# Kernel optimization log

Hardware: AMD Instinct MI355X
Metric: run time of the kernel (lower is better)

## Reference

```python
import jax, jax.numpy as jnp
import numpy as np

N_NODES = 100000
N_EDGES = 320000
DIM = 128
BN_EPS = 1e-5
AGG_EPS = 1e-6


def setup_inputs() -> dict:
    key = jax.random.key(0)
    ks = jax.random.split(key, 12)
    s = 1.0 / np.sqrt(DIM)
    inp = {
        "x": jax.random.normal(ks[0], (N_NODES, DIM), dtype=jnp.float32),
        "e": jax.random.normal(ks[1], (N_EDGES, DIM), dtype=jnp.float32),
        "edge_index": jax.random.randint(ks[2], (2, N_EDGES), 0, N_NODES, dtype=jnp.int32),
        "Wa": jax.random.normal(ks[3], (DIM, DIM), dtype=jnp.float32) * s,
        "ba": jnp.zeros((DIM,), dtype=jnp.float32),
        "Wb": jax.random.normal(ks[4], (DIM, DIM), dtype=jnp.float32) * s,
        "bb": jnp.zeros((DIM,), dtype=jnp.float32),
        "Wd": jax.random.normal(ks[5], (DIM, DIM), dtype=jnp.float32) * s,
        "bd": jnp.zeros((DIM,), dtype=jnp.float32),
        "We": jax.random.normal(ks[6], (DIM, DIM), dtype=jnp.float32) * s,
        "be": jnp.zeros((DIM,), dtype=jnp.float32),
        "gamma": jnp.ones((DIM,), dtype=jnp.float32),
        "beta": jnp.zeros((DIM,), dtype=jnp.float32),
    }
    return inp


def reference(x, e, edge_index, Wa, ba, Wb, bb, Wd, bd, We, be, gamma, beta):
    # PyG source_to_target flow: j = edge_index[0] (source), i = edge_index[1] (target)
    src = edge_index[0]
    dst = edge_index[1]

    Ax = x @ Wa + ba
    Bx = x @ Wb + bb
    Dx = x @ Wd + bd
    Ex = x @ We + be

    # message: e_ij = Dx_i + Ex_j ; sigma = sigmoid(e_ij)  [n_edges, out_dim]
    e_ij = Dx[dst] + Ex[src]
    sigma = jax.nn.sigmoid(e_ij)

    # aggregate: gated mean over incoming edges of each target node
    num = jax.ops.segment_sum(sigma * Bx[src], dst, num_segments=N_NODES)
    den = jax.ops.segment_sum(sigma, dst, num_segments=N_NODES)
    aggr = num / (den + AGG_EPS)

    # update + BatchNorm (training stats, biased var) + ReLU; dropout=0, residual=False
    h = Ax + aggr
    mean = jnp.mean(h, axis=0)
    var = jnp.mean(jnp.square(h - mean), axis=0)
    h_norm = (h - mean) * jax.lax.rsqrt(var + BN_EPS)
    x_out = jax.nn.relu(gamma * h_norm + beta)

    # edge output is raw e_ij (bn_edge_e is never applied in forward)
    return x_out, e_ij
```

## Files before the change

kernel.cpp:

```cpp
#include <hip/hip_runtime.h>
#include <hip/hip_bf16.h>
#include <stdint.h>

#define N_NODES 100000
#define N_EDGES 320000
#define DIM 128
#define AGG_EPS 1e-6f
#define BN_EPS 1e-5f
#define NODE_BLOCKS 2048
#define SCAN_BLOCKS 391

typedef float f32x4 __attribute__((ext_vector_type(4)));
typedef float f32x2 __attribute__((ext_vector_type(2)));
typedef __bf16 bf16x8 __attribute__((ext_vector_type(8)));

__device__ __forceinline__ uint32_t f2bf(float f) {
  union { float f; uint32_t u; } v; v.f = f;
  uint32_t u = v.u;
  return (u + 0x7fffu + ((u >> 16) & 1u)) >> 16;
}
__device__ __forceinline__ float bf2f(uint32_t h) {
  union { uint32_t u; float f; } v; v.u = h << 16;
  return v.f;
}

__device__ __forceinline__ void nt_store2(float* p, float a, float b) {
  f32x2 v = {a, b};
  __builtin_nontemporal_store(v, (f32x2*)p);
}


__global__ __launch_bounds__(256) void k_prep(
    const float* __restrict__ Wa, const float* __restrict__ ba,
    const float* __restrict__ Wb, const float* __restrict__ bb,
    const float* __restrict__ Wd, const float* __restrict__ bd,
    const float* __restrict__ We, const float* __restrict__ be,
    ushort* __restrict__ wt, float* __restrict__ biasc,
    uint4* __restrict__ cnt_zero) {
  __shared__ float tile[64][65];
  const int tid = threadIdx.x;
  const int b = blockIdx.x;
  const int sel = b >> 2, tr = (b >> 1) & 1, tc = b & 1;
  const float* W = (sel == 0) ? Wa : (sel == 1) ? Wb : (sel == 2) ? Wd : We;
#pragma unroll
  for (int i = 0; i < 16; ++i) {
    int idx = tid + 256 * i;
    int lr = idx >> 6, lc = idx & 63;
    tile[lr][lc] = W[(tr * 64 + lr) * 128 + tc * 64 + lc];
  }
  __syncthreads();
#pragma unroll
  for (int i = 0; i < 16; ++i) {
    int idx = tid + 256 * i;
    int oc = idx >> 6, ok = idx & 63;
    wt[(sel * 128 + tc * 64 + oc) * 128 + tr * 64 + ok] = (ushort)f2bf(tile[ok][oc]);
  }
  if (b == 0) {
    for (int t = tid; t < 512; t += 256) {
      int s2 = t >> 7;
      const float* bp = (s2 == 0) ? ba : (s2 == 1) ? bb : (s2 == 2) ? bd : be;
      biasc[t] = bp[t & 127];
    }
  }
  for (int j = b * 256 + tid; j < 25000; j += 16 * 256)
    cnt_zero[j] = make_uint4(0u, 0u, 0u, 0u);
}

__global__ __launch_bounds__(256) void k_gemm(
    const float* __restrict__ x, const ushort* __restrict__ wt,
    const float* __restrict__ biasc, ushort* __restrict__ abde) {
  __shared__ ushort As[128 * 128];
  __shared__ ushort Bs[64 * 128];
  const int tid = threadIdx.x;
  const int m0 = blockIdx.x * 128;

#pragma unroll
  for (int i = 0; i < 8; ++i) {
    int qid = tid + 256 * i;
    int row = qid >> 4, q = qid & 15;
    int gr = m0 + row;
    uint4 pk = make_uint4(0u, 0u, 0u, 0u);
    if (gr < N_NODES) {
      const float* s = x + (size_t)gr * 128 + q * 8;
      float4 f0 = *(const float4*)(s);
      float4 f1 = *(const float4*)(s + 4);
      pk.x = f2bf(f0.x) | (f2bf(f0.y) << 16);
      pk.y = f2bf(f0.z) | (f2bf(f0.w) << 16);
      pk.z = f2bf(f1.x) | (f2bf(f1.y) << 16);
      pk.w = f2bf(f1.z) | (f2bf(f1.w) << 16);
    }
    int byte = (row * 256 + q * 16) ^ ((row & 7) << 4);
    *(uint4*)((char*)As + byte) = pk;
  }
  __syncthreads();

  const int w = tid >> 6, lane = tid & 63;
  const int r = lane & 15, g = lane >> 4;

  bf16x8 afrag[2][4];
#pragma unroll
  for (int m = 0; m < 2; ++m)
#pragma unroll
    for (int kk = 0; kk < 4; ++kk) {
      int arow = w * 32 + m * 16 + r;
      int ab = (arow * 256 + kk * 64 + g * 16) ^ ((arow & 7) << 4);
      afrag[m][kk] = *(const bf16x8*)((const char*)As + ab);
    }

  const int ntpair[4][2] = {{2, 6}, {3, 7}, {0, 4}, {1, 5}};
  for (int ph = 0; ph < 4; ++ph) {
    f32x4 acc[2][2][4] = {};
#pragma unroll
    for (int t2 = 0; t2 < 2; ++t2) {
      if (ph | t2) __syncthreads();
      const int n0 = ntpair[ph][t2] * 64;
#pragma unroll
      for (int i = 0; i < 4; ++i) {
        int qid = tid + 256 * i;
        int row = qid >> 4, q = qid & 15;
        uint4 v = *(const uint4*)(wt + (n0 + row) * 128 + q * 8);
        int byte = (row * 256 + q * 16) ^ ((row & 7) << 4);
        *(uint4*)((char*)Bs + byte) = v;
      }
      __syncthreads();
#pragma unroll
      for (int kk = 0; kk < 4; ++kk) {
        bf16x8 bv[4];
#pragma unroll
        for (int n = 0; n < 4; ++n) {
          int brow = n * 16 + r;
          int bb = (brow * 256 + kk * 64 + g * 16) ^ ((brow & 7) << 4);
          bv[n] = *(const bf16x8*)((const char*)Bs + bb);
        }
#pragma unroll
        for (int m = 0; m < 2; ++m)
#pragma unroll
          for (int n = 0; n < 4; ++n)
            acc[t2][m][n] = __builtin_amdgcn_mfma_f32_16x16x32_bf16(
                afrag[m][kk], bv[n], acc[t2][m][n], 0, 0, 0);
      }
    }
#pragma unroll
    for (int t2 = 0; t2 < 2; ++t2) {
#pragma unroll
      for (int m = 0; m < 2; ++m) {
#pragma unroll
        for (int n = 0; n < 4; ++n) {
          int lc = t2 * 64 + n * 16 + r;
          float bsv = biasc[ntpair[ph][t2] * 64 + n * 16 + r];
#pragma unroll
          for (int q = 0; q < 4; ++q) {
            int row = w * 32 + m * 16 + g * 4 + q;
            As[row * 128 + (lc ^ (((row >> 2) & 3) << 4))] =
                (ushort)f2bf(acc[t2][m][n][q] + bsv);
          }
        }
      }
    }
    __syncthreads();
#pragma unroll
    for (int it = 0; it < 8; ++it) {
      int u = tid + 256 * it;
      int row = u >> 4, mq = u & 15;
      int xo = ((row >> 2) & 3) << 4;
      uint2 lo = *(const uint2*)&As[row * 128 + ((4 * mq) ^ xo)];
      uint2 hi = *(const uint2*)&As[row * 128 + ((64 + 4 * mq) ^ xo)];
      uint4 val = (ph < 2) ? make_uint4(hi.x, lo.x, hi.y, lo.y)
                           : make_uint4(lo.x, hi.x, lo.y, hi.y);
      int gr = m0 + row;
      if (gr < N_NODES)
        *(uint4*)((char*)abde + (size_t)gr * 1024 + (ph * 16 + mq) * 16) = val;
    }
  }
}

__global__ __launch_bounds__(256) void k_count(const int* __restrict__ dst,
                                               int* __restrict__ cnt) {
  int t = blockIdx.x * 256 + threadIdx.x;
  if (t < N_EDGES) atomicAdd(&cnt[dst[t]], 1);
}

__global__ __launch_bounds__(256) void k_bsum(const int* __restrict__ cnt,
                                              int* __restrict__ bsum2) {
  __shared__ int lds[256];
  int t = threadIdx.x;
  int i = blockIdx.x * 256 + t;
  lds[t] = (i < N_NODES) ? cnt[i] : 0;
  __syncthreads();
#pragma unroll
  for (int off = 128; off > 0; off >>= 1) {
    if (t < off) lds[t] += lds[t + off];
    __syncthreads();
  }
  if (t == 0) bsum2[blockIdx.x] = lds[0];
}

__global__ __launch_bounds__(256) void k_scan(const int* __restrict__ cnt,
                                              const int* __restrict__ bsum2,
                                              int* __restrict__ row_ptr,
                                              int* __restrict__ cursor) {
  __shared__ int ps[256];
  __shared__ int lds[256];
  __shared__ int boff_s;
  const int t = threadIdx.x;
  int a = (2 * t < SCAN_BLOCKS) ? bsum2[2 * t] : 0;
  int b = (2 * t + 1 < SCAN_BLOCKS) ? bsum2[2 * t + 1] : 0;
  ps[t] = a + b;
  __syncthreads();
  for (int off = 1; off < 256; off <<= 1) {
    int v = (t >= off) ? ps[t - off] : 0;
    __syncthreads();
    ps[t] += v;
    __syncthreads();
  }
  if (t == 0) {
    int b0 = blockIdx.x, p = b0 >> 1;
    int pre = (p > 0) ? ps[p - 1] : 0;
    if (b0 & 1) pre += bsum2[b0 - 1];
    boff_s = pre;
  }
  int i = blockIdx.x * 256 + t;
  int v = (i < N_NODES) ? cnt[i] : 0;
  lds[t] = v;
  __syncthreads();
  for (int off = 1; off < 256; off <<= 1) {
    int u = (t >= off) ? lds[t - off] : 0;
    __syncthreads();
    lds[t] += u;
    __syncthreads();
  }
  if (i < N_NODES) {
    int ex = boff_s + lds[t] - v;
    row_ptr[i] = ex;
    cursor[i] = ex;
  }
  if (blockIdx.x == 0 && t == 0) row_ptr[N_NODES] = N_EDGES;
}

__global__ __launch_bounds__(256) void k_scatter(const int* __restrict__ dst,
                                                 const int* __restrict__ srcArr,
                                                 int* __restrict__ cursor,
                                                 int* __restrict__ csr_eid,
                                                 int* __restrict__ csr_src) {
  int t = blockIdx.x * 256 + threadIdx.x;
  if (t < N_EDGES) {
    int d = dst[t];
    int s = srcArr[t];
    int pos = atomicAdd(&cursor[d], 1);
    csr_eid[pos] = t;
    csr_src[pos] = s;
  }
}

__global__ __launch_bounds__(256) void k_node(
    const ushort* __restrict__ abde, const int* __restrict__ row_ptr,
    const int* __restrict__ csr_eid, const int* __restrict__ csr_src,
    float* __restrict__ out_e, ushort* __restrict__ h,
    float* __restrict__ partials) {
  const int tid = threadIdx.x;
  const int lane = tid & 63;
  const int wid = (blockIdx.x << 2) | (tid >> 6);
  const int nw = NODE_BLOCKS * 4;
  float s0 = 0.f, s1 = 0.f, q0 = 0.f, q1 = 0.f;

  int i = wid;
  int k0 = 0, ke = 0;
  uint2 ad = make_uint2(0u, 0u);
  if (i < N_NODES) {
    k0 = row_ptr[i];
    ke = row_ptr[i + 1];
    ad = *(const uint2*)((const char*)abde + (size_t)i * 1024 + 512 + lane * 8);
  }
  while (i < N_NODES) {
    const int inext = i + nw;
    int nk0 = 0, nke = 0;
    uint2 nad = make_uint2(0u, 0u);
    if (inext < N_NODES) {
      nk0 = row_ptr[inext];
      nke = row_ptr[inext + 1];
      nad = *(const uint2*)((const char*)abde + (size_t)inext * 1024 + 512 + lane * 8);
    }
    float ax0 = bf2f(ad.x & 0xffffu), ax1 = bf2f(ad.x >> 16);
    float dx0 = bf2f(ad.y & 0xffffu), dx1 = bf2f(ad.y >> 16);
    float n0 = 0.f, n1 = 0.f, d0 = 0.f, d1 = 0.f;
    for (int base = k0; base < ke; base += 64) {
      const int cnt = min(64, ke - base);
      int eidv = 0, srcv = 0;
      if (lane < cnt) {
        eidv = csr_eid[base + lane];
        srcv = csr_src[base + lane];
      }
      int j = 0;
      for (; j + 2 <= cnt; j += 2) {
        int eA = __shfl(eidv, j),     sA = __shfl(srcv, j);
        int eB = __shfl(eidv, j + 1), sB = __shfl(srcv, j + 1);
        uint2 ebA = *(const uint2*)((const char*)abde + (size_t)sA * 1024 + lane * 8);
        uint2 ebB = *(const uint2*)((const char*)abde + (size_t)sB * 1024 + lane * 8);
        float e0 = dx0 + bf2f(ebA.x & 0xffffu);
        float e1 = dx1 + bf2f(ebA.x >> 16);
        nt_store2(out_e + (size_t)eA * 128 + 2 * lane, e0, e1);
        float sg0 = 1.f / (1.f + __expf(-e0));
        float sg1 = 1.f / (1.f + __expf(-e1));
        n0 += sg0 * bf2f(ebA.y & 0xffffu); n1 += sg1 * bf2f(ebA.y >> 16);
        d0 += sg0; d1 += sg1;
        float f0 = dx0 + bf2f(ebB.x & 0xffffu);
        float f1 = dx1 + bf2f(ebB.x >> 16);
        nt_store2(out_e + (size_t)eB * 128 + 2 * lane, f0, f1);
        float tg0 = 1.f / (1.f + __expf(-f0));
        float tg1 = 1.f / (1.f + __expf(-f1));
        n0 += tg0 * bf2f(ebB.y & 0xffffu); n1 += tg1 * bf2f(ebB.y >> 16);
        d0 += tg0; d1 += tg1;
      }
      if (j < cnt) {
        int eA = __shfl(eidv, j), sA = __shfl(srcv, j);
        uint2 ebA = *(const uint2*)((const char*)abde + (size_t)sA * 1024 + lane * 8);
        float e0 = dx0 + bf2f(ebA.x & 0xffffu);
        float e1 = dx1 + bf2f(ebA.x >> 16);
        nt_store2(out_e + (size_t)eA * 128 + 2 * lane, e0, e1);
        float sg0 = 1.f / (1.f + __expf(-e0));
        float sg1 = 1.f / (1.f + __expf(-e1));
        n0 += sg0 * bf2f(ebA.y & 0xffffu); n1 += sg1 * bf2f(ebA.y >> 16);
        d0 += sg0; d1 += sg1;
      }
    }
    float h0 = ax0 + n0 / (d0 + AGG_EPS);
    float h1 = ax1 + n1 / (d1 + AGG_EPS);
    *(uint32_t*)(h + (size_t)i * 128 + 2 * lane) = f2bf(h0) | (f2bf(h1) << 16);
    s0 += h0; s1 += h1; q0 += h0 * h0; q1 += h1 * h1;
    i = inext; k0 = nk0; ke = nke; ad = nad;
  }
  __shared__ float red[256 * 4];
  red[tid] = s0; red[256 + tid] = s1; red[512 + tid] = q0; red[768 + tid] = q1;
  __syncthreads();
  if (tid < 64) {
    float vs0 = red[tid] + red[tid + 64] + red[tid + 128] + red[tid + 192];
    float vs1 = red[256 + tid] + red[256 + tid + 64] + red[256 + tid + 128] + red[256 + tid + 192];
    float vq0 = red[512 + tid] + red[512 + tid + 64] + red[512 + tid + 128] + red[512 + tid + 192];
    float vq1 = red[768 + tid] + red[768 + tid + 64] + red[768 + tid + 128] + red[768 + tid + 192];
    float* p = partials + blockIdx.x * 256;
    p[2 * tid] = vs0;
    p[2 * tid + 1] = vs1;
    p[128 + 2 * tid] = vq0;
    p[128 + 2 * tid + 1] = vq1;
  }
}

__global__ __launch_bounds__(256) void k_stats1(const float* __restrict__ partials,
                                                float* __restrict__ out2) {
  int t = threadIdx.x, b = blockIdx.x;
  float s = 0.f;
#pragma unroll
  for (int j = 0; j < 32; ++j) s += partials[(b * 32 + j) * 256 + t];
  out2[b * 256 + t] = s;
}

__global__ __launch_bounds__(128) void k_stats2(const float* __restrict__ out2,
                                                float* __restrict__ stats) {
  int c = threadIdx.x;
  float s = 0.f, q = 0.f;
#pragma unroll
  for (int b = 0; b < 64; ++b) {
    s += out2[b * 256 + c];
    q += out2[b * 256 + 128 + c];
  }
  float mean = s * (1.f / (float)N_NODES);
  float var = q * (1.f / (float)N_NODES) - mean * mean;
  stats[c] = mean;
  stats[128 + c] = rsqrtf(var + BN_EPS);
}

__global__ __launch_bounds__(256) void k_final(const ushort* __restrict__ h,
    const float* __restrict__ gamma, const float* __restrict__ beta,
    const float* __restrict__ stats, float* __restrict__ out_x) {
  int idx = blockIdx.x * 256 + threadIdx.x;
  int c = (idx & 15) * 8;
  uint4 hv = *(const uint4*)(h + idx * 8);
  uint32_t hw[4] = {hv.x, hv.y, hv.z, hv.w};
  float out[8];
#pragma unroll
  for (int j = 0; j < 8; ++j) {
    uint32_t u = (j & 1) ? (hw[j >> 1] >> 16) : (hw[j >> 1] & 0xffffu);
    float hf = bf2f(u);
    int cc = c + j;
    float v = gamma[cc] * (hf - stats[cc]) * stats[128 + cc] + beta[cc];
    out[j] = fmaxf(v, 0.f);
  }
  f32x4 v0 = {out[0], out[1], out[2], out[3]};
  f32x4 v1 = {out[4], out[5], out[6], out[7]};
  __builtin_nontemporal_store(v0, (f32x4*)(out_x + idx * 8));
  __builtin_nontemporal_store(v1, (f32x4*)(out_x + idx * 8 + 4));
}

extern "C" void kernel_launch(void* const* d_in, const int* in_sizes, int n_in,
                              void* d_out, int out_size, void* d_ws, size_t ws_size,
                              hipStream_t stream) {
  const float* x = (const float*)d_in[0];
  const int* edge_index = (const int*)d_in[2];
  const float* Wa = (const float*)d_in[3];
  const float* ba = (const float*)d_in[4];
  const float* Wb = (const float*)d_in[5];
  const float* bb = (const float*)d_in[6];
  const float* Wd = (const float*)d_in[7];
  const float* bd = (const float*)d_in[8];
  const float* We = (const float*)d_in[9];
  const float* be = (const float*)d_in[10];
  const float* gamma = (const float*)d_in[11];
  const float* beta = (const float*)d_in[12];

  const int* src = edge_index;
  const int* dst = edge_index + N_EDGES;

  char* w = (char*)d_ws;
  ushort* wt      = (ushort*)(w);
  float*  biasc   = (float*)(w + 131072);
  ushort* abde    = (ushort*)(w + 133120);
  ushort* hbuf    = (ushort*)(w + 102533120);
  int*    cnt     = (int*)(w + 128133120);
  int*    row_ptr = (int*)(w + 128533120);
  int*    cursor  = (int*)(w + 128933248);
  int*    csr_eid = (int*)(w + 129333248);
  float*  partials= (float*)(w + 130613248);
  float*  stats   = (float*)(w + 132710400);

  int*   bsum2 = (int*)partials;
  float* out2  = (float*)cnt;

  float* out_x = (float*)d_out;
  float* out_e = out_x + (size_t)N_NODES * DIM;
  int* csr_src = (int*)out_x;

  k_prep<<<16, 256, 0, stream>>>(Wa, ba, Wb, bb, Wd, bd, We, be, wt, biasc, (uint4*)cnt);
  k_gemm<<<782, 256, 0, stream>>>(x, wt, biasc, abde);
  k_count<<<(N_EDGES + 255) / 256, 256, 0, stream>>>(dst, cnt);
  k_bsum<<<SCAN_BLOCKS, 256, 0, stream>>>(cnt, bsum2);
  k_scan<<<SCAN_BLOCKS, 256, 0, stream>>>(cnt, bsum2, row_ptr, cursor);
  k_scatter<<<(N_EDGES + 255) / 256, 256, 0, stream>>>(dst, src, cursor, csr_eid, csr_src);
  k_node<<<NODE_BLOCKS, 256, 0, stream>>>(abde, row_ptr, csr_eid, csr_src, out_e, hbuf, partials);
  k_stats1<<<64, 256, 0, stream>>>(partials, out2);
  k_stats2<<<1, 128, 0, stream>>>(out2, stats);
  k_final<<<6250, 256, 0, stream>>>(hbuf, gamma, beta, stats, out_x);
}
```

Measured before the change: 176.0 us.

## Fuse CSR build and BN stats kernels to cut launch count

Edge counting moves into extra blocks of the GEMM launch so both run concurrently. Block-sum, scan and scatter are merged into one cooperative kernel that uses grid-wide syncs. The two stats kernels become one, where the last-arriving block (found through an atomic ticket) computes mean and rstd. This removes several kernel launches and their gaps, but adds grid-sync overhead and requires all 1250 cooperative blocks to be co-resident.

```diff
diff --git a/kernel.cpp b/kernel.cpp
--- a/kernel.cpp
+++ b/kernel.cpp
@@ -1,6 +1,9 @@
 #include <hip/hip_runtime.h>
 #include <hip/hip_bf16.h>
+#include <hip/hip_cooperative_groups.h>
 #include <stdint.h>
+
+namespace cg = cooperative_groups;
 
 #define N_NODES 100000
 #define N_EDGES 320000
@@ -9,6 +12,8 @@
 #define BN_EPS 1e-5f
 #define NODE_BLOCKS 2048
 #define SCAN_BLOCKS 391
+#define GEMM_BLOCKS 782
+#define EDGE_BLOCKS 1250
 
 typedef float f32x4 __attribute__((ext_vector_type(4)));
 typedef float f32x2 __attribute__((ext_vector_type(2)));
@@ -23,7 +28,6 @@
   union { uint32_t u; float f; } v; v.u = h << 16;
   return v.f;
 }
-
 __device__ __forceinline__ void nt_store2(float* p, float a, float b) {
   f32x2 v = {a, b};
   __builtin_nontemporal_store(v, (f32x2*)p);
@@ -36,7 +40,7 @@
     const float* __restrict__ Wd, const float* __restrict__ bd,
     const float* __restrict__ We, const float* __restrict__ be,
     ushort* __restrict__ wt, float* __restrict__ biasc,
-    uint4* __restrict__ cnt_zero) {
+    uint4* __restrict__ cnt_zero, int* __restrict__ done) {
   __shared__ float tile[64][65];
   const int tid = threadIdx.x;
   const int b = blockIdx.x;
@@ -61,18 +65,27 @@
       const float* bp = (s2 == 0) ? ba : (s2 == 1) ? bb : (s2 == 2) ? bd : be;
       biasc[t] = bp[t & 127];
     }
+    if (tid == 0) *done = 0;
   }
   for (int j = b * 256 + tid; j < 25000; j += 16 * 256)
     cnt_zero[j] = make_uint4(0u, 0u, 0u, 0u);
 }
 
-__global__ __launch_bounds__(256) void k_gemm(
+__global__ __launch_bounds__(256) void k_gemm_count(
     const float* __restrict__ x, const ushort* __restrict__ wt,
-    const float* __restrict__ biasc, ushort* __restrict__ abde) {
+    const float* __restrict__ biasc, ushort* __restrict__ abde,
+    const int* __restrict__ dst, int* __restrict__ cnt) {
   __shared__ ushort As[128 * 128];
   __shared__ ushort Bs[64 * 128];
   const int tid = threadIdx.x;
-  const int m0 = blockIdx.x * 128;
+  const int bid = blockIdx.x;
+
+  if (bid >= GEMM_BLOCKS) {
+    int e = (bid - GEMM_BLOCKS) * 256 + tid;
+    if (e < N_EDGES) atomicAdd(&cnt[dst[e]], 1);
+    return;
+  }
+  const int m0 = bid * 128;
 
 #pragma unroll
   for (int i = 0; i < 8; ++i) {
@@ -174,80 +187,73 @@
   }
 }
 
-__global__ __launch_bounds__(256) void k_count(const int* __restrict__ dst,
-                                               int* __restrict__ cnt) {
-  int t = blockIdx.x * 256 + threadIdx.x;
-  if (t < N_EDGES) atomicAdd(&cnt[dst[t]], 1);
-}
-
-__global__ __launch_bounds__(256) void k_bsum(const int* __restrict__ cnt,
-                                              int* __restrict__ bsum2) {
-  __shared__ int lds[256];
-  int t = threadIdx.x;
-  int i = blockIdx.x * 256 + t;
-  lds[t] = (i < N_NODES) ? cnt[i] : 0;
-  __syncthreads();
-#pragma unroll
-  for (int off = 128; off > 0; off >>= 1) {
-    if (t < off) lds[t] += lds[t + off];
-    __syncthreads();
-  }
-  if (t == 0) bsum2[blockIdx.x] = lds[0];
-}
-
-__global__ __launch_bounds__(256) void k_scan(const int* __restrict__ cnt,
-                                              const int* __restrict__ bsum2,
-                                              int* __restrict__ row_ptr,
-                                              int* __restrict__ cursor) {
+__global__ __launch_bounds__(256) void k_csr(
+    const int* __restrict__ dst, const int* __restrict__ srcArr,
+    const int* __restrict__ cnt, int* __restrict__ bsum2,
+    int* __restrict__ row_ptr, int* __restrict__ cursor,
+    int* __restrict__ csr_eid, int* __restrict__ csr_src) {
+  cg::grid_group grid = cg::this_grid();
   __shared__ int ps[256];
   __shared__ int lds[256];
   __shared__ int boff_s;
   const int t = threadIdx.x;
-  int a = (2 * t < SCAN_BLOCKS) ? bsum2[2 * t] : 0;
-  int b = (2 * t + 1 < SCAN_BLOCKS) ? bsum2[2 * t + 1] : 0;
-  ps[t] = a + b;
-  __syncthreads();
-  for (int off = 1; off < 256; off <<= 1) {
-    int v = (t >= off) ? ps[t - off] : 0;
+  const int b = blockIdx.x;
+
+  if (b < SCAN_BLOCKS) {
+    int i = b * 256 + t;
+    lds[t] = (i < N_NODES) ? cnt[i] : 0;
     __syncthreads();
-    ps[t] += v;
+#pragma unroll
+    for (int off = 128; off > 0; off >>= 1) {
+      if (t < off) lds[t] += lds[t + off];
+      __syncthreads();
+    }
+    if (t == 0) bsum2[b] = lds[0];
+  }
+  grid.sync();
+
+  if (b < SCAN_BLOCKS) {
+    int a = (2 * t < SCAN_BLOCKS) ? bsum2[2 * t] : 0;
+    int bb = (2 * t + 1 < SCAN_BLOCKS) ? bsum2[2 * t + 1] : 0;
+    ps[t] = a + bb;
     __syncthreads();
-  }
-  if (t == 0) {
-    int b0 = blockIdx.x, p = b0 >> 1;
-    int pre = (p > 0) ? ps[p - 1] : 0;
-    if (b0 & 1) pre += bsum2[b0 - 1];
-    boff_s = pre;
-  }
-  int i = blockIdx.x * 256 + t;
-  int v = (i < N_NODES) ? cnt[i] : 0;
-  lds[t] = v;
-  __syncthreads();
-  for (int off = 1; off < 256; off <<= 1) {
-    int u = (t >= off) ? lds[t - off] : 0;
+    for (int off = 1; off < 256; off <<= 1) {
+      int v = (t >= off) ? ps[t - off] : 0;
+      __syncthreads();
+      ps[t] += v;
+      __syncthreads();
+    }
+    if (t == 0) {
+      int p = b >> 1;
+      int pre = (p > 0) ? ps[p - 1] : 0;
+      if (b & 1) pre += bsum2[b - 1];
+      boff_s = pre;
+    }
+    int i = b * 256 + t;
+    int v = (i < N_NODES) ? cnt[i] : 0;
+    lds[t] = v;
     __syncthreads();
-    lds[t] += u;
-    __syncthreads();
-  }
-  if (i < N_NODES) {
-    int ex = boff_s + lds[t] - v;
-    row_ptr[i] = ex;
-    cursor[i] = ex;
-  }
-  if (blockIdx.x == 0 && t == 0) row_ptr[N_NODES] = N_EDGES;
-}
-
-__global__ __launch_bounds__(256) void k_scatter(const int* __restrict__ dst,
-                                                 const int* __restrict__ srcArr,
-                                                 int* __restrict__ cursor,
-                                                 int* __restrict__ csr_eid,
-                                                 int* __restrict__ csr_src) {
-  int t = blockIdx.x * 256 + threadIdx.x;
-  if (t < N_EDGES) {
-    int d = dst[t];
-    int s = srcArr[t];
+    for (int off = 1; off < 256; off <<= 1) {
+      int u = (t >= off) ? lds[t - off] : 0;
+      __syncthreads();
+      lds[t] += u;
+      __syncthreads();
+    }
+    if (i < N_NODES) {
+      int ex = boff_s + lds[t] - v;
+      row_ptr[i] = ex;
+      cursor[i] = ex;
+    }
+    if (b == 0 && t == 0) row_ptr[N_NODES] = N_EDGES;
+  }
+  grid.sync();
+
+  int e = b * 256 + t;
+  if (e < N_EDGES) {
+    int d = dst[e];
+    int s = srcArr[e];
     int pos = atomicAdd(&cursor[d], 1);
-    csr_eid[pos] = t;
+    csr_eid[pos] = e;
     csr_src[pos] = s;
   }
 }
@@ -345,28 +351,31 @@
   }
 }
 
-__global__ __launch_bounds__(256) void k_stats1(const float* __restrict__ partials,
-                                                float* __restrict__ out2) {
-  int t = threadIdx.x, b = blockIdx.x;
+__global__ __launch_bounds__(256) void k_stats(const float* __restrict__ partials,
+                                               float* __restrict__ out2,
+                                               float* __restrict__ stats,
+                                               int* __restrict__ done) {
+  const int t = threadIdx.x, b = blockIdx.x;
   float s = 0.f;
 #pragma unroll
   for (int j = 0; j < 32; ++j) s += partials[(b * 32 + j) * 256 + t];
   out2[b * 256 + t] = s;
-}
-
-__global__ __launch_bounds__(128) void k_stats2(const float* __restrict__ out2,
-                                                float* __restrict__ stats) {
-  int c = threadIdx.x;
-  float s = 0.f, q = 0.f;
-#pragma unroll
-  for (int b = 0; b < 64; ++b) {
-    s += out2[b * 256 + c];
-    q += out2[b * 256 + 128 + c];
-  }
-  float mean = s * (1.f / (float)N_NODES);
-  float var = q * (1.f / (float)N_NODES) - mean * mean;
-  stats[c] = mean;
-  stats[128 + c] = rsqrtf(var + BN_EPS);
+  __threadfence();
+  __shared__ int ticket;
+  if (t == 0) ticket = atomicAdd(done, 1);
+  __syncthreads();
+  if (ticket == 63 && t < 128) {
+    float ss = 0.f, qq = 0.f;
+#pragma unroll
+    for (int bb = 0; bb < 64; ++bb) {
+      ss += out2[bb * 256 + t];
+      qq += out2[bb * 256 + 128 + t];
+    }
+    float mean = ss * (1.f / (float)N_NODES);
+    float var = qq * (1.f / (float)N_NODES) - mean * mean;
+    stats[t] = mean;
+    stats[128 + t] = rsqrtf(var + BN_EPS);
+  }
 }
 
 __global__ __launch_bounds__(256) void k_final(const ushort* __restrict__ h,
@@ -424,19 +433,22 @@
 
   int*   bsum2 = (int*)partials;
   float* out2  = (float*)cnt;
+  int*   done  = row_ptr + 100001;
 
   float* out_x = (float*)d_out;
   float* out_e = out_x + (size_t)N_NODES * DIM;
   int* csr_src = (int*)out_x;
 
-  k_prep<<<16, 256, 0, stream>>>(Wa, ba, Wb, bb, Wd, bd, We, be, wt, biasc, (uint4*)cnt);
-  k_gemm<<<782, 256, 0, stream>>>(x, wt, biasc, abde);
-  k_count<<<(N_EDGES + 255) / 256, 256, 0, stream>>>(dst, cnt);
-  k_bsum<<<SCAN_BLOCKS, 256, 0, stream>>>(cnt, bsum2);
-  k_scan<<<SCAN_BLOCKS, 256, 0, stream>>>(cnt, bsum2, row_ptr, cursor);
-  k_scatter<<<(N_EDGES + 255) / 256, 256, 0, stream>>>(dst, src, cursor, csr_eid, csr_src);
+  k_prep<<<16, 256, 0, stream>>>(Wa, ba, Wb, bb, Wd, bd, We, be, wt, biasc,
+                                 (uint4*)cnt, done);
+  k_gemm_count<<<GEMM_BLOCKS + EDGE_BLOCKS, 256, 0, stream>>>(x, wt, biasc, abde, dst, cnt);
+  {
+    void* args[] = {(void*)&dst, (void*)&src, (void*)&cnt, (void*)&bsum2,
+                    (void*)&row_ptr, (void*)&cursor, (void*)&csr_eid, (void*)&csr_src};
+    hipLaunchCooperativeKernel((const void*)k_csr, dim3(EDGE_BLOCKS), dim3(256),
+                               args, 0, stream);
+  }
   k_node<<<NODE_BLOCKS, 256, 0, stream>>>(abde, row_ptr, csr_eid, csr_src, out_e, hbuf, partials);
-  k_stats1<<<64, 256, 0, stream>>>(partials, out2);
-  k_stats2<<<1, 128, 0, stream>>>(out2, stats);
+  k_stats<<<64, 256, 0, stream>>>(partials, out2, stats, done);
   k_final<<<6250, 256, 0, stream>>>(hbuf, gamma, beta, stats, out_x);
 }
```

Result: slower. 439.0 us (+149.5%).
